# Kernel tuning notes

Hardware: AMD Instinct MI355X
Metric: run time of the kernel (lower is better)

Reference implementation:

```python
import jax, jax.numpy as jnp
import numpy as np

N_SAMPLES = 2048
N_CHANNELS = 4096
N_COMPONENTS = 4


def setup_inputs() -> dict:
    key = jax.random.key(0)
    k1, k2, k3, k4 = jax.random.split(key, 4)
    inputs = jax.random.uniform(k1, (N_SAMPLES, N_CHANNELS), jnp.float32)
    # keras 'uniform' init (small values), NonNeg-constrained -> small positive
    components = jax.random.uniform(k2, (N_COMPONENTS, N_CHANNELS), jnp.float32) * 0.05
    contributions = jax.random.uniform(k3, (N_SAMPLES, N_COMPONENTS), jnp.float32) * 0.05
    # shifts in roughly [-4, 4] channels to exercise the soft-shift path
    shift = (jax.random.uniform(k4, (N_SAMPLES, N_COMPONENTS), jnp.float32) - 0.5) * 8.0
    return {"inputs": inputs, "components": components,
            "contributions": contributions, "shift": shift}


def reference(inputs, components, contributions, shift):
    """fit_shift=True path of SingleModalFactorization.

    Original builds, per sample and component, a C x C matrix
    coeff[i, j] = clip(1 - |(j - i) - shift|, 0, 1) and matmuls it with the
    component vector. That coefficient matrix has at most two nonzeros per
    row: j = i + floor(shift) with weight (1 - frac) and j = i + floor(shift) + 1
    with weight frac (zero outside [0, C)). We compute exactly that banded
    2-tap linear interpolation -- identical math, O(C) instead of O(C^2).
    """
    S, C = inputs.shape
    K = components.shape[0]
    m = jnp.floor(shift)                       # (S, K) integer part
    f = (shift - m)[:, :, None]                # (S, K, 1) fractional part
    mi = m.astype(jnp.int32)[:, :, None]       # (S, K, 1)
    ch = jnp.arange(C, dtype=jnp.int32)[None, None, :]  # (1, 1, C)
    idx0 = ch + mi                             # (S, K, C)
    idx1 = idx0 + 1
    v0 = (idx0 >= 0) & (idx0 < C)
    v1 = (idx1 >= 0) & (idx1 < C)
    kk = jnp.arange(K, dtype=jnp.int32)[None, :, None]
    g0 = jnp.where(v0, components[kk, jnp.clip(idx0, 0, C - 1)], 0.0)
    g1 = jnp.where(v1, components[kk, jnp.clip(idx1, 0, C - 1)], 0.0)
    shifted = (1.0 - f) * g0 + f * g1          # (S, K, C) shifted components
    # weight each shifted component by its per-sample contribution and sum
    return jnp.einsum('skc,sk->sc', shifted, contributions)
```

## Files before the change

### kernel.cpp

```cpp
#include <hip/hip_runtime.h>

constexpr int S = 2048;
constexpr int C = 4096;
constexpr int K = 4;

constexpr int BLOCK = 256;
constexpr int VEC = 4;
constexpr int CHUNK = BLOCK * VEC;
constexpr int CHUNKS_PER_SAMPLE = C / CHUNK;

typedef float f4u __attribute__((ext_vector_type(4), aligned(4)));

__global__ __launch_bounds__(BLOCK) void smf_kernel(
    const float* __restrict__ comp,
    const float* __restrict__ contrib,
    const float* __restrict__ shift,
    float* __restrict__ out)
{
    const int s  = blockIdx.x >> 2;
    const int c0 = (blockIdx.x & 3) * CHUNK;
    const int c  = c0 + (int)threadIdx.x * VEC;

    float w0[K], w1[K];
    int   m[K];
    int mmin = 1 << 30, mmax = -(1 << 30);
#pragma unroll
    for (int k = 0; k < K; ++k) {
        const float sh = shift[s * K + k];
        const float ct = contrib[s * K + k];
        const float mf = floorf(sh);
        const float f  = sh - mf;
        m[k]  = (int)mf;
        w0[k] = ct * (1.0f - f);
        w1[k] = ct * f;
        mmin = min(mmin, m[k]);
        mmax = max(mmax, m[k]);
    }

    float4 acc = make_float4(0.f, 0.f, 0.f, 0.f);

    const bool fast = (c + mmin >= 0) && (c + VEC - 1 + mmax + 1 < C);
    if (fast) {
#pragma unroll
        for (int k = 0; k < K; ++k) {
            const float* p = comp + k * C + c + m[k];
            const f4u  v = *(const f4u*)p;
            const float e = p[4];
            acc.x += w0[k] * v.x + w1[k] * v.y;
            acc.y += w0[k] * v.y + w1[k] * v.z;
            acc.z += w0[k] * v.z + w1[k] * v.w;
            acc.w += w0[k] * v.w + w1[k] * e;
        }
    } else {
        float a[VEC] = {0.f, 0.f, 0.f, 0.f};
#pragma unroll
        for (int j = 0; j < VEC; ++j) {
            const int cc = c + j;
#pragma unroll
            for (int k = 0; k < K; ++k) {
                const int i0 = cc + m[k];
                const int i1 = i0 + 1;
                const float g0 = (i0 >= 0 && i0 < C) ? comp[k * C + i0] : 0.f;
                const float g1 = (i1 >= 0 && i1 < C) ? comp[k * C + i1] : 0.f;
                a[j] += w0[k] * g0 + w1[k] * g1;
            }
        }
        acc = make_float4(a[0], a[1], a[2], a[3]);
    }

    *(float4*)(out + s * C + c) = acc;
}

extern "C" void kernel_launch(void* const* d_in, const int* in_sizes, int n_in,
                              void* d_out, int out_size, void* d_ws, size_t ws_size,
                              hipStream_t stream) {
    const float* comp    = (const float*)d_in[1];
    const float* contrib = (const float*)d_in[2];
    const float* shift   = (const float*)d_in[3];
    float* out = (float*)d_out;

    const int grid = S * CHUNKS_PER_SAMPLE;
    smf_kernel<<<grid, BLOCK, 0, stream>>>(comp, contrib, shift, out);
}
```

Before: 95.87 us.

## Process a whole sample per block with 16 outputs per thread and nontemporal stores

Each block now covers one full sample row, with every thread producing 16 consecutive outputs instead of 4. This cuts the grid to one block per sample, spreads the per-sample shift and weight setup over more work, and lets each thread reuse one loaded window per component across 16 outputs. Output writes use nontemporal stores so the large write stream bypasses cache retention. In exchange each thread holds more registers, the grid has fewer blocks, and stores are no longer fully coalesced per instruction because adjacent lanes write 64 bytes apart.

```diff
diff --git a/kernel.cpp b/kernel.cpp
--- a/kernel.cpp
+++ b/kernel.cpp
@@ -5,11 +5,10 @@
 constexpr int K = 4;
 
 constexpr int BLOCK = 256;
-constexpr int VEC = 4;
-constexpr int CHUNK = BLOCK * VEC;
-constexpr int CHUNKS_PER_SAMPLE = C / CHUNK;
+constexpr int VEC = 16;
 
 typedef float f4u __attribute__((ext_vector_type(4), aligned(4)));
+typedef float f4n __attribute__((ext_vector_type(4)));
 
 __global__ __launch_bounds__(BLOCK) void smf_kernel(
     const float* __restrict__ comp,
@@ -17,9 +16,8 @@
     const float* __restrict__ shift,
     float* __restrict__ out)
 {
-    const int s  = blockIdx.x >> 2;
-    const int c0 = (blockIdx.x & 3) * CHUNK;
-    const int c  = c0 + (int)threadIdx.x * VEC;
+    const int s = blockIdx.x;
+    const int c = (int)threadIdx.x * VEC;
 
     float w0[K], w1[K];
     int   m[K];
@@ -37,22 +35,28 @@
         mmax = max(mmax, m[k]);
     }
 
-    float4 acc = make_float4(0.f, 0.f, 0.f, 0.f);
+    float acc[VEC];
+#pragma unroll
+    for (int j = 0; j < VEC; ++j) acc[j] = 0.f;
 
-    const bool fast = (c + mmin >= 0) && (c + VEC - 1 + mmax + 1 < C);
+    const bool fast = (c + mmin >= 0) && (c + VEC + mmax < C);
     if (fast) {
 #pragma unroll
         for (int k = 0; k < K; ++k) {
             const float* p = comp + k * C + c + m[k];
-            const f4u  v = *(const f4u*)p;
-            const float e = p[4];
-            acc.x += w0[k] * v.x + w1[k] * v.y;
-            acc.y += w0[k] * v.y + w1[k] * v.z;
-            acc.z += w0[k] * v.z + w1[k] * v.w;
-            acc.w += w0[k] * v.w + w1[k] * e;
+            float v[VEC + 1];
+#pragma unroll
+            for (int q = 0; q < VEC / 4; ++q) {
+                const f4u t = *(const f4u*)(p + 4 * q);
+                v[4 * q + 0] = t.x; v[4 * q + 1] = t.y;
+                v[4 * q + 2] = t.z; v[4 * q + 3] = t.w;
+            }
+            v[VEC] = p[VEC];
+#pragma unroll
+            for (int j = 0; j < VEC; ++j)
+                acc[j] += w0[k] * v[j] + w1[k] * v[j + 1];
         }
     } else {
-        float a[VEC] = {0.f, 0.f, 0.f, 0.f};
 #pragma unroll
         for (int j = 0; j < VEC; ++j) {
             const int cc = c + j;
@@ -62,13 +66,18 @@
                 const int i1 = i0 + 1;
                 const float g0 = (i0 >= 0 && i0 < C) ? comp[k * C + i0] : 0.f;
                 const float g1 = (i1 >= 0 && i1 < C) ? comp[k * C + i1] : 0.f;
-                a[j] += w0[k] * g0 + w1[k] * g1;
+                acc[j] += w0[k] * g0 + w1[k] * g1;
             }
         }
-        acc = make_float4(a[0], a[1], a[2], a[3]);
     }
 
-    *(float4*)(out + s * C + c) = acc;
+    float* op = out + s * C + c;
+#pragma unroll
+    for (int q = 0; q < VEC / 4; ++q) {
+        f4n st = { acc[4 * q + 0], acc[4 * q + 1],
+                   acc[4 * q + 2], acc[4 * q + 3] };
+        __builtin_nontemporal_store(st, (f4n*)(op + 4 * q));
+    }
 }
 
 extern "C" void kernel_launch(void* const* d_in, const int* in_sizes, int n_in,
@@ -79,6 +88,5 @@
     const float* shift   = (const float*)d_in[3];
     float* out = (float*)d_out;
 
-    const int grid = S * CHUNKS_PER_SAMPLE;
-    smf_kernel<<<grid, BLOCK, 0, stream>>>(comp, contrib, shift, out);
+    smf_kernel<<<S, BLOCK, 0, stream>>>(comp, contrib, shift, out);
 }
```

Result: slower. 106.7 us (+11.3%).
